# Optimization experiments

Measured on AMD Instinct MI355X. Metric: run time of the kernel, lower is better.

The kernel has to match this reference:

```python
import jax, jax.numpy as jnp
import numpy as np

B, T, INPUT_DIM, EMBED_DIM = 64, 512, 512, 256


def _lstm_dir(x, mask, k, r, b):
    """Masked unidirectional LSTM (Keras semantics: masked steps carry prev h/c).
    x: [B,T,D], mask: [B,T] bool, k: [D,4U], r: [U,4U], b: [4U]. Returns [B,T,U]."""
    Bx = x.shape[0]
    U = r.shape[0]
    # Precompute input projection once for all timesteps (gate order: i,f,g,o)
    xz = jnp.einsum('btd,dk->btk', x, k) + b          # [B,T,4U]
    xz_t = jnp.swapaxes(xz, 0, 1)                     # [T,B,4U]
    mask_t = jnp.swapaxes(mask, 0, 1)                 # [T,B]
    h0 = jnp.zeros((Bx, U), x.dtype)
    c0 = jnp.zeros((Bx, U), x.dtype)

    def step(carry, inp):
        h, c = carry
        z_x, m = inp
        z = z_x + h @ r                               # [B,4U]
        i, f, g, o = jnp.split(z, 4, axis=-1)
        i = jax.nn.sigmoid(i)
        f = jax.nn.sigmoid(f)
        g = jnp.tanh(g)
        o = jax.nn.sigmoid(o)
        c_new = f * c + i * g
        h_new = o * jnp.tanh(c_new)
        m = m[:, None]
        h2 = jnp.where(m, h_new, h)                   # carry state through masked steps
        c2 = jnp.where(m, c_new, c)
        return (h2, c2), h2

    _, hs = jax.lax.scan(step, (h0, c0), (xz_t, mask_t))
    return jnp.swapaxes(hs, 0, 1)                     # [B,T,U]


def _bilstm_sum(x, mask, kf, rf, bf, kb, rb, bb):
    fwd = _lstm_dir(x, mask, kf, rf, bf)
    # Keras Bidirectional: reverse input and mask, run, reverse output back
    bwd = _lstm_dir(x[:, ::-1], mask[:, ::-1], kb, rb, bb)[:, ::-1]
    return fwd + bwd                                  # merge_mode='sum'


def _lstm_params(key, d_in, units):
    k1, k2, k3 = jax.random.split(key, 3)
    kernel = jax.random.normal(k1, (d_in, 4 * units), jnp.float32) / np.sqrt(d_in)
    rec = jax.random.normal(k2, (units, 4 * units), jnp.float32) / np.sqrt(units)
    bias = jnp.concatenate([
        jnp.zeros((units,), jnp.float32),
        jnp.ones((units,), jnp.float32),              # unit_forget_bias
        jnp.zeros((2 * units,), jnp.float32),
    ])
    return kernel, rec, bias


def setup_inputs() -> dict:
    key = jax.random.key(0)
    ks = jax.random.split(key, 6)
    sequences = jax.random.normal(ks[0], (B, T, INPUT_DIM), jnp.float32)
    sizes = jax.random.randint(ks[1], (B,), 0, T, jnp.int32)
    enc_kf, enc_rf, enc_bf = _lstm_params(ks[2], INPUT_DIM, EMBED_DIM)
    enc_kb, enc_rb, enc_bb = _lstm_params(ks[3], INPUT_DIM, EMBED_DIM)
    dec_kf, dec_rf, dec_bf = _lstm_params(ks[4], EMBED_DIM, INPUT_DIM)
    dec_kb, dec_rb, dec_bb = _lstm_params(ks[5], EMBED_DIM, INPUT_DIM)
    return {
        'sequences': sequences, 'sizes': sizes,
        'enc_kf': enc_kf, 'enc_rf': enc_rf, 'enc_bf': enc_bf,
        'enc_kb': enc_kb, 'enc_rb': enc_rb, 'enc_bb': enc_bb,
        'dec_kf': dec_kf, 'dec_rf': dec_rf, 'dec_bf': dec_bf,
        'dec_kb': dec_kb, 'dec_rb': dec_rb, 'dec_bb': dec_bb,
    }


def reference(sequences, sizes,
              enc_kf, enc_rf, enc_bf, enc_kb, enc_rb, enc_bb,
              dec_kf, dec_rf, dec_bf, dec_kb, dec_rb, dec_bb):
    mask = jnp.arange(sequences.shape[1])[None, :] < sizes[:, None]   # [B,T]
    x = _bilstm_sum(sequences, mask, enc_kf, enc_rf, enc_bf, enc_kb, enc_rb, enc_bb)
    x = _bilstm_sum(x, mask, dec_kf, dec_rf, dec_bf, dec_kb, dec_rb, dec_bb)
    return x
```

## Files before the change

### kernel.cpp

```cpp
#include <hip/hip_runtime.h>
#include <stdint.h>

using short8 = __attribute__((ext_vector_type(8))) short;
using f32x4  = __attribute__((ext_vector_type(4))) float;

#define DEV static __device__ __forceinline__

DEV unsigned short f2bf(float f){
  unsigned u = __builtin_bit_cast(unsigned, f);
  u = (u + 0x7FFFu + ((u >> 16) & 1u)) >> 16;
  return (unsigned short)u;
}
DEV float sigm(float x){
  float e = __builtin_amdgcn_exp2f(-1.4426950408889634f * x);
  return __builtin_amdgcn_rcpf(1.0f + e);
}
DEV float tanh_(float x){
  float e = __builtin_amdgcn_exp2f(2.885390081777927f * x);
  return 1.0f - 2.0f * __builtin_amdgcn_rcpf(e + 1.0f);
}


__global__ void k_f32_to_bf16(const float* __restrict__ in, unsigned short* __restrict__ out, int n){
  int stride = gridDim.x * blockDim.x * 4;
  for (int i = (blockIdx.x * blockDim.x + threadIdx.x) * 4; i < n; i += stride){
    float4 v = *(const float4*)(in + i);
    ushort4 o4;
    o4.x = f2bf(v.x); o4.y = f2bf(v.y); o4.z = f2bf(v.z); o4.w = f2bf(v.w);
    *(ushort4*)(out + i) = o4;
  }
}

__global__ void k_add_bf16(const float* __restrict__ a, const float* __restrict__ b,
                           unsigned short* __restrict__ out, int n){
  int stride = gridDim.x * blockDim.x * 4;
  for (int i = (blockIdx.x * blockDim.x + threadIdx.x) * 4; i < n; i += stride){
    float4 va = *(const float4*)(a + i);
    float4 vb = *(const float4*)(b + i);
    ushort4 o4;
    o4.x = f2bf(va.x + vb.x); o4.y = f2bf(va.y + vb.y);
    o4.z = f2bf(va.z + vb.z); o4.w = f2bf(va.w + vb.w);
    *(ushort4*)(out + i) = o4;
  }
}

__global__ void k_add_f32(float* __restrict__ o, const float* __restrict__ b, int n){
  int stride = gridDim.x * blockDim.x * 4;
  for (int i = (blockIdx.x * blockDim.x + threadIdx.x) * 4; i < n; i += stride){
    float4 vo = *(const float4*)(o + i);
    float4 vb = *(const float4*)(b + i);
    vo.x += vb.x; vo.y += vb.y; vo.z += vb.z; vo.w += vb.w;
    *(float4*)(o + i) = vo;
  }
}

__global__ void k_pack(const float* __restrict__ k0, const float* __restrict__ r0,
                       const float* __restrict__ k1, const float* __restrict__ r1,
                       unsigned short* __restrict__ out, int E, int KX, int U){
  int n = 2 * E;
  int stride = gridDim.x * blockDim.x;
  for (int i = blockIdx.x * blockDim.x + threadIdx.x; i < n; i += stride){
    int d = i / E, r = i % E;
    const float* Km = d ? k1 : k0;
    const float* Rm = d ? r1 : r0;
    int j    = r & 7;  int q = r >> 3;
    int lane = q & 63; q >>= 6;
    int nt   = q & 3;  q >>= 2;
    int kt   = q % 6;  q /= 6;
    int w    = q & 3;  int wg = q >> 2;
    int k    = (w*6 + kt)*32 + ((lane >> 4) << 3) + j;
    int col  = nt * U + wg*16 + (lane & 15);
    float v  = (k < KX) ? Km[(size_t)k * (4*U) + col]
                        : Rm[(size_t)(k - KX) * (4*U) + col];
    out[i] = f2bf(v);
  }
}

template<int KX, int U, int WGS>
__global__ __launch_bounds__(256, 1)
void lstm_rec(const unsigned short* __restrict__ xab,
              const unsigned short* __restrict__ packedB,
              const float* __restrict__ bias_f,
              const float* __restrict__ bias_b,
              const int*   __restrict__ sizes,
              unsigned short* __restrict__ hbuf,
              unsigned int*  __restrict__ counters,
              float* __restrict__ out_f,
              float* __restrict__ out_b)
{
  constexpr int KTW = 6;
  constexpr int T   = 512;

  const int tid  = threadIdx.x;
  const int w    = tid >> 6;
  const int lane = tid & 63;
  const int dir  = (blockIdx.x >= WGS) ? 1 : 0;
  const int wg   = dir ? (int)blockIdx.x - WGS : (int)blockIdx.x;

  const unsigned short* pB = packedB + (size_t)dir * ((size_t)WGS*4*KTW*4*512)
                                     + (size_t)((wg*4 + w)*KTW)*4*512;
  unsigned short* hb  = hbuf + (size_t)dir * (2*64*U);
  unsigned int*   cnt = counters + dir * 32;
  const float* bias = dir ? bias_b : bias_f;
  float* outp       = dir ? out_b : out_f;

  const bool has_h = ((w*KTW + KTW - 1) * 32) >= KX;

  short8 bfr[KTW][4];
  #pragma unroll
  for (int kt = 0; kt < KTW; ++kt)
    #pragma unroll
    for (int nt = 0; nt < 4; ++nt)
      bfr[kt][nt] = *(const short8*)(pB + ((kt*4 + nt)*512) + lane*8);

  const int u_l = tid & 15;
  const int rb  = (tid >> 4) * 4;
  const int ug  = wg*16 + u_l;
  float bz[4]; int sz[4];
  #pragma unroll
  for (int g = 0; g < 4; ++g) bz[g] = bias[g*U + ug];
  #pragma unroll
  for (int r = 0; r < 4; ++r) sz[r] = sizes[rb + r];
  float c[4]    = {0.f,0.f,0.f,0.f};
  float hreg[4] = {0.f,0.f,0.f,0.f};

  __shared__ float part[4][64][68];

  const int arow  = lane & 15;
  const int kgrp  = (lane >> 4) * 8;
  const int rquad = (lane >> 4) * 4;

  short8 areg[KTW][4];
  {
    const int t0 = dir ? T - 1 : 0;
    #pragma unroll
    for (int kt = 0; kt < KTW; ++kt){
      const int kg = (w*KTW + kt) * 32;
      if (kg < KX){
        #pragma unroll
        for (int mt = 0; mt < 4; ++mt)
          areg[kt][mt] = *(const short8*)(xab + ((size_t)((mt*16 + arow)*T + t0))*KX + (kg + kgrp));
      }
    }
  }

  for (int s = 0; s < T; ++s){
    const int t   = dir ? (T - 1 - s) : s;
    const int par = s & 1;

    f32x4 acc[4][4];
    #pragma unroll
    for (int mt = 0; mt < 4; ++mt)
      #pragma unroll
      for (int nt = 0; nt < 4; ++nt)
        acc[mt][nt] = (f32x4){0.f, 0.f, 0.f, 0.f};

    #pragma unroll
    for (int kt = 0; kt < KTW; ++kt){
      const int kg = (w*KTW + kt) * 32;
      if (kg < KX){
        #pragma unroll
        for (int mt = 0; mt < 4; ++mt)
          #pragma unroll
          for (int nt = 0; nt < 4; ++nt)
            acc[mt][nt] = __builtin_amdgcn_mfma_f32_16x16x32_bf16(areg[kt][mt], bfr[kt][nt], acc[mt][nt], 0, 0, 0);
      }
    }

    if (s > 0){
      if (has_h){
        const unsigned tgt = (unsigned)WGS * (unsigned)s;
        for (;;){
          unsigned v = __hip_atomic_load(cnt, __ATOMIC_RELAXED, __HIP_MEMORY_SCOPE_AGENT);
          if (v >= tgt) break;
          __builtin_amdgcn_s_sleep(1);
        }
        __builtin_amdgcn_sched_barrier(0);
        #pragma unroll
        for (int kt = 0; kt < KTW; ++kt){
          const int kg = (w*KTW + kt) * 32;
          if (kg >= KX){
            #pragma unroll
            for (int mt = 0; mt < 4; ++mt){
              const unsigned long long* hp = (const unsigned long long*)
                  (hb + (size_t)par*64*U + (size_t)(mt*16 + arow)*U + (kg - KX + kgrp));
              ulonglong2 u;
              u.x = __hip_atomic_load(hp,     __ATOMIC_RELAXED, __HIP_MEMORY_SCOPE_AGENT);
              u.y = __hip_atomic_load(hp + 1, __ATOMIC_RELAXED, __HIP_MEMORY_SCOPE_AGENT);
              areg[kt][mt] = __builtin_bit_cast(short8, u);
            }
          }
        }
        #pragma unroll
        for (int kt = 0; kt < KTW; ++kt){
          const int kg = (w*KTW + kt) * 32;
          if (kg >= KX){
            #pragma unroll
            for (int mt = 0; mt < 4; ++mt)
              #pragma unroll
              for (int nt = 0; nt < 4; ++nt)
                acc[mt][nt] = __builtin_amdgcn_mfma_f32_16x16x32_bf16(areg[kt][mt], bfr[kt][nt], acc[mt][nt], 0, 0, 0);
          }
        }
      }
    }

    #pragma unroll
    for (int mt = 0; mt < 4; ++mt)
      #pragma unroll
      for (int nt = 0; nt < 4; ++nt)
        *(f32x4*)&part[w][nt*16 + arow][mt*16 + rquad] = acc[mt][nt];

    __syncthreads();

    f32x4 zg[4];
    #pragma unroll
    for (int g = 0; g < 4; ++g){
      const int cb = g*16 + u_l;
      f32x4 v = *(const f32x4*)&part[0][cb][rb];
      #pragma unroll
      for (int ww = 1; ww < 4; ++ww)
        v += *(const f32x4*)&part[ww][cb][rb];
      zg[g] = v;
    }

    #pragma unroll
    for (int r = 0; r < 4; ++r){
      float ig = sigm (zg[0][r] + bz[0]);
      float fg = sigm (zg[1][r] + bz[1]);
      float gg = tanh_(zg[2][r] + bz[2]);
      float og = sigm (zg[3][r] + bz[3]);
      float cn = fg * c[r] + ig * gg;
      float hn = og * tanh_(cn);
      bool m  = (t < sz[r]);
      c[r] = m ? cn : c[r];
      float h = m ? hn : hreg[r];
      hreg[r] = h;
      __hip_atomic_store(&hb[(size_t)(par ^ 1)*64*U + (size_t)(rb + r)*U + ug],
                         (unsigned short)f2bf(h),
                         __ATOMIC_RELAXED, __HIP_MEMORY_SCOPE_AGENT);
    }

    __syncthreads();

    if (s != T - 1){
      if (tid == 0) atomicAdd(cnt, 1u);
    }

    #pragma unroll
    for (int r = 0; r < 4; ++r)
      outp[((size_t)(rb + r)*T + t)*U + ug] = hreg[r];

    if (s != T - 1){
      const int tn = dir ? t - 1 : t + 1;
      #pragma unroll
      for (int kt = 0; kt < KTW; ++kt){
        const int kg = (w*KTW + kt) * 32;
        if (kg < KX){
          #pragma unroll
          for (int mt = 0; mt < 4; ++mt)
            areg[kt][mt] = *(const short8*)(xab + ((size_t)((mt*16 + arow)*T + tn))*KX + (kg + kgrp));
        }
      }
    }
  }
}


extern "C" void kernel_launch(void* const* d_in, const int* in_sizes, int n_in,
                              void* d_out, int out_size, void* d_ws, size_t ws_size,
                              hipStream_t stream){
  const float* x      = (const float*)d_in[0];
  const int*   sizes  = (const int*)  d_in[1];
  const float* enc_kf = (const float*)d_in[2];
  const float* enc_rf = (const float*)d_in[3];
  const float* enc_bf = (const float*)d_in[4];
  const float* enc_kb = (const float*)d_in[5];
  const float* enc_rb = (const float*)d_in[6];
  const float* enc_bb = (const float*)d_in[7];
  const float* dec_kf = (const float*)d_in[8];
  const float* dec_rf = (const float*)d_in[9];
  const float* dec_bf = (const float*)d_in[10];
  const float* dec_kb = (const float*)d_in[11];
  const float* dec_rb = (const float*)d_in[12];
  const float* dec_bb = (const float*)d_in[13];
  float* out = (float*)d_out;
  char*  ws  = (char*)d_ws;

  const size_t o_xbf   = 0;
  const size_t o_esum  = o_xbf   + 33554432ull;
  const size_t o_pBe   = o_esum  + 16777216ull;
  const size_t o_pBd   = o_pBe   + 3145728ull;
  const size_t o_hfe   = o_pBd   + 6291456ull;
  const size_t o_hbe   = o_hfe   + 33554432ull;
  const size_t o_hbd   = o_hbe   + 33554432ull;
  const size_t o_hbufe = o_hbd   + 67108864ull;
  const size_t o_hbufd = o_hbufe + 131072ull;
  const size_t o_cnte  = o_hbufd + 262144ull;
  const size_t o_cntd  = o_cnte  + 4096ull;
  const size_t total   = o_cntd  + 4096ull;
  if (ws_size < total) return;

  unsigned short* xbf   = (unsigned short*)(ws + o_xbf);
  unsigned short* esum  = (unsigned short*)(ws + o_esum);
  unsigned short* pBe   = (unsigned short*)(ws + o_pBe);
  unsigned short* pBd   = (unsigned short*)(ws + o_pBd);
  float*          hfe   = (float*)(ws + o_hfe);
  float*          hbe   = (float*)(ws + o_hbe);
  float*          hbd   = (float*)(ws + o_hbd);
  unsigned short* hbufe = (unsigned short*)(ws + o_hbufe);
  unsigned short* hbufd = (unsigned short*)(ws + o_hbufd);
  unsigned int*   cnte  = (unsigned int*)(ws + o_cnte);
  unsigned int*   cntd  = (unsigned int*)(ws + o_cntd);

  hipMemsetAsync(ws + o_cnte, 0, 8192ull, stream);

  k_f32_to_bf16<<<2048, 256, 0, stream>>>(x, xbf, 64*512*512);

  k_pack<<<2048, 256, 0, stream>>>(enc_kf, enc_rf, enc_kb, enc_rb, pBe, 786432, 512, 256);
  k_pack<<<2048, 256, 0, stream>>>(dec_kf, dec_rf, dec_kb, dec_rb, pBd, 1572864, 256, 512);

  lstm_rec<512, 256, 16><<<32, 256, 0, stream>>>(xbf, pBe, enc_bf, enc_bb, sizes,
                                                 hbufe, cnte, hfe, hbe);
  k_add_bf16<<<2048, 256, 0, stream>>>(hfe, hbe, esum, 64*512*256);

  lstm_rec<256, 512, 32><<<64, 256, 0, stream>>>(esum, pBd, dec_bf, dec_bb, sizes,
                                                 hbufd, cntd, out, hbd);
  k_add_f32<<<2048, 256, 0, stream>>>(out, hbd, 64*512*512);
}
```

Before: 5.580 ms.

## Hoist encoder input projection into parallel GEMM and run recurrence per-block with LDS

The encoder's input projection moves out of the recurrent loop into a separate fully parallel MFMA GEMM that writes bf16 gate pre-activations in a transposed layout. The encoder recurrence becomes a new kernel in which each of 8 blocks owns 16 batch rows and one direction, keeps the whole recurrent matrix in registers, and exchanges h through LDS with a local barrier. This removes the cross-workgroup atomic spin-wait per timestep. It costs a large extra workspace buffer (~128MB xz), bf16 rounding of the precomputed gates, and only 8 active CUs during the encoder recurrence. A fallback path keeps the old pipeline when the workspace is too small.

```diff
diff --git a/kernel.cpp b/kernel.cpp
--- a/kernel.cpp
+++ b/kernel.cpp
@@ -3,6 +3,7 @@
 
 using short8 = __attribute__((ext_vector_type(8))) short;
 using f32x4  = __attribute__((ext_vector_type(4))) float;
+typedef unsigned long long ull;
 
 #define DEV static __device__ __forceinline__
 
@@ -11,6 +12,9 @@
   u = (u + 0x7FFFu + ((u >> 16) & 1u)) >> 16;
   return (unsigned short)u;
 }
+DEV float bf2f(unsigned short v){
+  return __builtin_bit_cast(float, ((unsigned)v) << 16);
+}
 DEV float sigm(float x){
   float e = __builtin_amdgcn_exp2f(-1.4426950408889634f * x);
   return __builtin_amdgcn_rcpf(1.0f + e);
@@ -18,6 +22,16 @@
 DEV float tanh_(float x){
   float e = __builtin_amdgcn_exp2f(2.885390081777927f * x);
   return 1.0f - 2.0f * __builtin_amdgcn_rcpf(e + 1.0f);
+}
+DEV void bar_lds(){
+  __builtin_amdgcn_sched_barrier(0);
+  asm volatile("s_waitcnt lgkmcnt(0)" ::: "memory");
+  __builtin_amdgcn_s_barrier();
+  __builtin_amdgcn_sched_barrier(0);
+}
+DEV void colmap_e(int colp, int& g, int& u){
+  int w = colp >> 7, r = colp & 127, nt = r >> 4, l = r & 15;
+  g = nt >> 1; u = w*32 + ((nt & 1) << 4) + l;
 }
 
 
@@ -41,6 +55,20 @@
     o4.x = f2bf(va.x + vb.x); o4.y = f2bf(va.y + vb.y);
     o4.z = f2bf(va.z + vb.z); o4.w = f2bf(va.w + vb.w);
     *(ushort4*)(out + i) = o4;
+  }
+}
+
+__global__ void k_add_bb(const unsigned short* __restrict__ a, const unsigned short* __restrict__ b,
+                         unsigned short* __restrict__ out, int n){
+  int stride = gridDim.x * blockDim.x * 8;
+  for (int i = (blockIdx.x * blockDim.x + threadIdx.x) * 8; i < n; i += stride){
+    short8 va = *(const short8*)(a + i);
+    short8 vb = *(const short8*)(b + i);
+    short8 o;
+    #pragma unroll
+    for (int j = 0; j < 8; ++j)
+      o[j] = (short)f2bf(bf2f((unsigned short)va[j]) + bf2f((unsigned short)vb[j]));
+    *(short8*)(out + i) = o;
   }
 }
 
@@ -76,6 +104,210 @@
   }
 }
 
+__global__ void k_pack_ge(const float* __restrict__ kf, const float* __restrict__ kb,
+                          unsigned short* __restrict__ out){
+  int n = 2 * 524288;
+  int stride = gridDim.x * blockDim.x;
+  for (int i = blockIdx.x * blockDim.x + threadIdx.x; i < n; i += stride){
+    int j    = i & 7;
+    int lane = (i >> 3) & 63;
+    int nt   = (i >> 9) & 3;
+    int kt   = (i >> 11) & 3;
+    int w    = (i >> 13) & 3;
+    int ct   = (i >> 15) & 15;
+    int dir  = i >> 19;
+    int k    = (w*4 + kt)*32 + ((lane >> 4) << 3) + j;
+    int colp = ct*64 + nt*16 + (lane & 15);
+    int g, u; colmap_e(colp, g, u);
+    const float* K = dir ? kb : kf;
+    out[i] = f2bf(K[(size_t)k * 1024 + g*256 + u]);
+  }
+}
+
+__global__ void k_pack_re(const float* __restrict__ rf, const float* __restrict__ rb,
+                          unsigned short* __restrict__ out){
+  int n = 2 * 262144;
+  int stride = gridDim.x * blockDim.x;
+  for (int i = blockIdx.x * blockDim.x + threadIdx.x; i < n; i += stride){
+    int j    = i & 7;
+    int lane = (i >> 3) & 63;
+    int nt   = (i >> 9) & 7;
+    int kt   = (i >> 12) & 7;
+    int w    = (i >> 15) & 7;
+    int dir  = i >> 18;
+    int k    = kt*32 + ((lane >> 4) << 3) + j;
+    int colp = w*128 + nt*16 + (lane & 15);
+    int g, u; colmap_e(colp, g, u);
+    const float* R = dir ? rb : rf;
+    out[i] = f2bf(R[(size_t)k * 1024 + g*256 + u]);
+  }
+}
+
+__global__ __launch_bounds__(256, 1)
+void k_gemm_xz(const unsigned short* __restrict__ xab,
+               const unsigned short* __restrict__ pBg,
+               unsigned short* __restrict__ xzt){
+  const int tid  = threadIdx.x;
+  const int w    = tid >> 6;
+  const int lane = tid & 63;
+  const int ct   = blockIdx.x & 15;
+  const int t    = (blockIdx.x >> 4) & 511;
+  const int dir  = blockIdx.x >> 13;
+
+  short8 bfr[4][4];
+  #pragma unroll
+  for (int kt = 0; kt < 4; ++kt)
+    #pragma unroll
+    for (int nt = 0; nt < 4; ++nt)
+      bfr[kt][nt] = *(const short8*)(pBg + (size_t)((((dir*16 + ct)*4 + w)*4 + kt)*4 + nt)*512 + lane*8);
+
+  const int arow = lane & 15;
+  const int kgrp = (lane >> 4) * 8;
+  const int rquad = (lane >> 4) * 4;
+
+  f32x4 acc[4][4];
+  #pragma unroll
+  for (int mt = 0; mt < 4; ++mt)
+    #pragma unroll
+    for (int nt = 0; nt < 4; ++nt)
+      acc[mt][nt] = (f32x4){0.f,0.f,0.f,0.f};
+
+  #pragma unroll
+  for (int kt = 0; kt < 4; ++kt){
+    const int kg = (w*4 + kt)*32;
+    #pragma unroll
+    for (int mt = 0; mt < 4; ++mt){
+      const int row = mt*16 + arow;
+      short8 a = *(const short8*)(xab + ((size_t)(row*512 + t))*512 + kg + kgrp);
+      #pragma unroll
+      for (int nt = 0; nt < 4; ++nt)
+        acc[mt][nt] = __builtin_amdgcn_mfma_f32_16x16x32_bf16(a, bfr[kt][nt], acc[mt][nt], 0, 0, 0);
+    }
+  }
+
+  __shared__ float part[4][64][68];
+  #pragma unroll
+  for (int mt = 0; mt < 4; ++mt)
+    #pragma unroll
+    for (int nt = 0; nt < 4; ++nt)
+      *(f32x4*)&part[w][nt*16 + arow][mt*16 + rquad] = acc[mt][nt];
+
+  __syncthreads();
+
+  const int cl = tid & 63;
+  const int rq = (tid >> 6) * 16;
+  unsigned short ov[16];
+  #pragma unroll
+  for (int q = 0; q < 4; ++q){
+    f32x4 v = *(const f32x4*)&part[0][cl][rq + q*4];
+    #pragma unroll
+    for (int ww = 1; ww < 4; ++ww)
+      v += *(const f32x4*)&part[ww][cl][rq + q*4];
+    #pragma unroll
+    for (int r = 0; r < 4; ++r) ov[q*4 + r] = f2bf(v[r]);
+  }
+  size_t base = ((size_t)(dir*1024 + ct*64 + cl))*32768 + (size_t)t*64 + rq;
+  *(short8*)(xzt + base)     = *(short8*)&ov[0];
+  *(short8*)(xzt + base + 8) = *(short8*)&ov[8];
+}
+
+__global__ __launch_bounds__(512, 1)
+void k_enc_rec(const unsigned short* __restrict__ xzt,
+               const unsigned short* __restrict__ pBr,
+               const float* __restrict__ bias_f,
+               const float* __restrict__ bias_b,
+               const int*   __restrict__ sizes,
+               unsigned short* __restrict__ out_f,
+               unsigned short* __restrict__ out_b){
+  constexpr int T = 512;
+  const int tid   = threadIdx.x;
+  const int w     = tid >> 6;
+  const int lane  = tid & 63;
+  const int l15   = lane & 15;
+  const int dir   = (int)blockIdx.x >> 2;
+  const int rbase = ((int)blockIdx.x & 3) * 16;
+
+  short8 bfr[8][8];
+  #pragma unroll
+  for (int kt = 0; kt < 8; ++kt)
+    #pragma unroll
+    for (int nt = 0; nt < 8; ++nt)
+      bfr[kt][nt] = *(const short8*)(pBr + (size_t)(((dir*8 + w)*8 + kt)*8 + nt)*512 + lane*8);
+
+  const float* bias = dir ? bias_b : bias_f;
+  unsigned short* outp = dir ? out_b : out_f;
+
+  float bz[2][4];
+  #pragma unroll
+  for (int us = 0; us < 2; ++us){
+    const int u = w*32 + us*16 + l15;
+    #pragma unroll
+    for (int g = 0; g < 4; ++g) bz[us][g] = bias[g*256 + u];
+  }
+  int sz[4];
+  #pragma unroll
+  for (int r2 = 0; r2 < 4; ++r2) sz[r2] = sizes[rbase + (lane >> 4)*4 + r2];
+
+  float c[2][4], hv[2][4];
+  #pragma unroll
+  for (int us = 0; us < 2; ++us)
+    #pragma unroll
+    for (int r2 = 0; r2 < 4; ++r2){ c[us][r2] = 0.f; hv[us][r2] = 0.f; }
+
+  __shared__ unsigned short hl[2][16][264];
+  for (int i = tid; i < 16*264; i += 512) ((unsigned short*)hl[0])[i] = 0;
+  __syncthreads();
+
+  const size_t xzdir = (size_t)dir * 1024 * 32768;
+
+  for (int s = 0; s < T; ++s){
+    const int t   = dir ? (T - 1 - s) : s;
+    const int par = s & 1;
+
+    f32x4 acc[8];
+    #pragma unroll
+    for (int nt = 0; nt < 8; ++nt){
+      const int colp = w*128 + nt*16 + l15;
+      const unsigned short* p = xzt + xzdir + (size_t)colp*32768 + (size_t)t*64 + rbase + ((lane >> 4) << 2);
+      ushort4 xv = *(const ushort4*)p;
+      acc[nt] = (f32x4){bf2f(xv.x), bf2f(xv.y), bf2f(xv.z), bf2f(xv.w)};
+    }
+
+    #pragma unroll
+    for (int kt = 0; kt < 8; ++kt){
+      short8 a = *(const short8*)&hl[par][l15][kt*32 + ((lane >> 4) << 3)];
+      #pragma unroll
+      for (int nt = 0; nt < 8; ++nt)
+        acc[nt] = __builtin_amdgcn_mfma_f32_16x16x32_bf16(a, bfr[kt][nt], acc[nt], 0, 0, 0);
+    }
+
+    #pragma unroll
+    for (int us = 0; us < 2; ++us){
+      const int u = w*32 + us*16 + l15;
+      #pragma unroll
+      for (int r2 = 0; r2 < 4; ++r2){
+        float zi = acc[0 + us][r2] + bz[us][0];
+        float zf = acc[2 + us][r2] + bz[us][1];
+        float zg = acc[4 + us][r2] + bz[us][2];
+        float zo = acc[6 + us][r2] + bz[us][3];
+        float ig = sigm(zi), fg = sigm(zf), gg = tanh_(zg), og = sigm(zo);
+        float cn = fg * c[us][r2] + ig * gg;
+        float hn = og * tanh_(cn);
+        bool m = (t < sz[r2]);
+        c[us][r2] = m ? cn : c[us][r2];
+        float h = m ? hn : hv[us][r2];
+        hv[us][r2] = h;
+        unsigned short hb16 = f2bf(h);
+        const int rloc = (lane >> 4)*4 + r2;
+        hl[par ^ 1][rloc][u] = hb16;
+        outp[((size_t)((rbase + rloc)*512) + t)*256 + u] = hb16;
+      }
+    }
+
+    bar_lds();
+  }
+}
+
 template<int KX, int U, int WGS>
 __global__ __launch_bounds__(256, 1)
 void lstm_rec(const unsigned short* __restrict__ xab,
@@ -130,7 +362,7 @@
   const int kgrp  = (lane >> 4) * 8;
   const int rquad = (lane >> 4) * 4;
 
-  short8 areg[KTW][4];
+  short8 xreg[KTW][4];
   {
     const int t0 = dir ? T - 1 : 0;
     #pragma unroll
@@ -139,7 +371,7 @@
       if (kg < KX){
         #pragma unroll
         for (int mt = 0; mt < 4; ++mt)
-          areg[kt][mt] = *(const short8*)(xab + ((size_t)((mt*16 + arow)*T + t0))*KX + (kg + kgrp));
+          xreg[kt][mt] = *(const short8*)(xab + ((size_t)((mt*16 + arow)*T + t0))*KX + (kg + kgrp));
       }
     }
   }
@@ -163,43 +395,33 @@
         for (int mt = 0; mt < 4; ++mt)
           #pragma unroll
           for (int nt = 0; nt < 4; ++nt)
-            acc[mt][nt] = __builtin_amdgcn_mfma_f32_16x16x32_bf16(areg[kt][mt], bfr[kt][nt], acc[mt][nt], 0, 0, 0);
+            acc[mt][nt] = __builtin_amdgcn_mfma_f32_16x16x32_bf16(xreg[kt][mt], bfr[kt][nt], acc[mt][nt], 0, 0, 0);
       }
     }
 
-    if (s > 0){
-      if (has_h){
-        const unsigned tgt = (unsigned)WGS * (unsigned)s;
-        for (;;){
-          unsigned v = __hip_atomic_load(cnt, __ATOMIC_RELAXED, __HIP_MEMORY_SCOPE_AGENT);
-          if (v >= tgt) break;
-          __builtin_amdgcn_s_sleep(1);
-        }
-        __builtin_amdgcn_sched_barrier(0);
-        #pragma unroll
-        for (int kt = 0; kt < KTW; ++kt){
-          const int kg = (w*KTW + kt) * 32;
-          if (kg >= KX){
+    if (s > 0 && has_h){
+      const unsigned tgt = (unsigned)WGS * (unsigned)s;
+      for (;;){
+        unsigned v = __hip_atomic_load(cnt, __ATOMIC_RELAXED, __HIP_MEMORY_SCOPE_AGENT);
+        if (v >= tgt) break;
+        __builtin_amdgcn_s_sleep(1);
+      }
+      __builtin_amdgcn_sched_barrier(0);
+      #pragma unroll
+      for (int kt = 0; kt < KTW; ++kt){
+        const int kg = (w*KTW + kt) * 32;
+        if (kg >= KX){
+          #pragma unroll
+          for (int mt = 0; mt < 4; ++mt){
+            const ull* hp = (const ull*)
+                (hb + (size_t)par*64*U + (size_t)(mt*16 + arow)*U + (kg - KX + kgrp));
+            ulonglong2 u;
+            u.x = __hip_atomic_load(hp,     __ATOMIC_RELAXED, __HIP_MEMORY_SCOPE_AGENT);
+            u.y = __hip_atomic_load(hp + 1, __ATOMIC_RELAXED, __HIP_MEMORY_SCOPE_AGENT);
+            short8 a = __builtin_bit_cast(short8, u);
             #pragma unroll
-            for (int mt = 0; mt < 4; ++mt){
-              const unsigned long long* hp = (const unsigned long long*)
-                  (hb + (size_t)par*64*U + (size_t)(mt*16 + arow)*U + (kg - KX + kgrp));
-              ulonglong2 u;
-              u.x = __hip_atomic_load(hp,     __ATOMIC_RELAXED, __HIP_MEMORY_SCOPE_AGENT);
-              u.y = __hip_atomic_load(hp + 1, __ATOMIC_RELAXED, __HIP_MEMORY_SCOPE_AGENT);
-              areg[kt][mt] = __builtin_bit_cast(short8, u);
-            }
-          }
-        }
-        #pragma unroll
-        for (int kt = 0; kt < KTW; ++kt){
-          const int kg = (w*KTW + kt) * 32;
-          if (kg >= KX){
-            #pragma unroll
-            for (int mt = 0; mt < 4; ++mt)
-              #pragma unroll
-              for (int nt = 0; nt < 4; ++nt)
-                acc[mt][nt] = __builtin_amdgcn_mfma_f32_16x16x32_bf16(areg[kt][mt], bfr[kt][nt], acc[mt][nt], 0, 0, 0);
+            for (int nt = 0; nt < 4; ++nt)
+              acc[mt][nt] = __builtin_amdgcn_mfma_f32_16x16x32_bf16(a, bfr[kt][nt], acc[mt][nt], 0, 0, 0);
           }
         }
       }
@@ -259,7 +481,7 @@
         if (kg < KX){
           #pragma unroll
           for (int mt = 0; mt < 4; ++mt)
-            areg[kt][mt] = *(const short8*)(xab + ((size_t)((mt*16 + arow)*T + tn))*KX + (kg + kgrp));
+            xreg[kt][mt] = *(const short8*)(xab + ((size_t)((mt*16 + arow)*T + tn))*KX + (kg + kgrp));
         }
       }
     }
@@ -287,44 +509,75 @@
   float* out = (float*)d_out;
   char*  ws  = (char*)d_ws;
 
-  const size_t o_xbf   = 0;
-  const size_t o_esum  = o_xbf   + 33554432ull;
-  const size_t o_pBe   = o_esum  + 16777216ull;
-  const size_t o_pBd   = o_pBe   + 3145728ull;
-  const size_t o_hfe   = o_pBd   + 6291456ull;
-  const size_t o_hbe   = o_hfe   + 33554432ull;
-  const size_t o_hbd   = o_hbe   + 33554432ull;
-  const size_t o_hbufe = o_hbd   + 67108864ull;
-  const size_t o_hbufd = o_hbufe + 131072ull;
-  const size_t o_cnte  = o_hbufd + 262144ull;
-  const size_t o_cntd  = o_cnte  + 4096ull;
-  const size_t total   = o_cntd  + 4096ull;
-  if (ws_size < total) return;
-
-  unsigned short* xbf   = (unsigned short*)(ws + o_xbf);
-  unsigned short* esum  = (unsigned short*)(ws + o_esum);
-  unsigned short* pBe   = (unsigned short*)(ws + o_pBe);
-  unsigned short* pBd   = (unsigned short*)(ws + o_pBd);
-  float*          hfe   = (float*)(ws + o_hfe);
-  float*          hbe   = (float*)(ws + o_hbe);
-  float*          hbd   = (float*)(ws + o_hbd);
-  unsigned short* hbufe = (unsigned short*)(ws + o_hbufe);
-  unsigned short* hbufd = (unsigned short*)(ws + o_hbufd);
-  unsigned int*   cnte  = (unsigned int*)(ws + o_cnte);
-  unsigned int*   cntd  = (unsigned int*)(ws + o_cntd);
-
-  hipMemsetAsync(ws + o_cnte, 0, 8192ull, stream);
-
-  k_f32_to_bf16<<<2048, 256, 0, stream>>>(x, xbf, 64*512*512);
-
-  k_pack<<<2048, 256, 0, stream>>>(enc_kf, enc_rf, enc_kb, enc_rb, pBe, 786432, 512, 256);
-  k_pack<<<2048, 256, 0, stream>>>(dec_kf, dec_rf, dec_kb, dec_rb, pBd, 1572864, 256, 512);
-
-  lstm_rec<512, 256, 16><<<32, 256, 0, stream>>>(xbf, pBe, enc_bf, enc_bb, sizes,
-                                                 hbufe, cnte, hfe, hbe);
-  k_add_bf16<<<2048, 256, 0, stream>>>(hfe, hbe, esum, 64*512*256);
-
-  lstm_rec<256, 512, 32><<<64, 256, 0, stream>>>(esum, pBd, dec_bf, dec_bb, sizes,
-                                                 hbufd, cntd, out, hbd);
-  k_add_f32<<<2048, 256, 0, stream>>>(out, hbd, 64*512*512);
-}
+  const size_t o_xbf  = 0;
+  const size_t o_esum = o_xbf  + 33554432ull;
+  const size_t o_pBd  = o_esum + 16777216ull;
+  const size_t o_ehf  = o_pBd  + 6291456ull;
+  const size_t o_ehb  = o_ehf  + 16777216ull;
+  const size_t o_hbd  = o_ehb  + 16777216ull;
+  const size_t o_hbufd= o_hbd  + 67108864ull;
+  const size_t o_cntd = o_hbufd+ 262144ull;
+  const size_t o_pBg  = o_cntd + 4096ull;
+  const size_t o_pBr  = o_pBg  + 2097152ull;
+  const size_t o_xzt  = o_pBr  + 1048576ull;
+  const size_t NEWTOT = o_xzt  + 134217728ull;
+
+  unsigned short* xbf  = (unsigned short*)(ws + o_xbf);
+  unsigned short* esum = (unsigned short*)(ws + o_esum);
+  unsigned short* pBd  = (unsigned short*)(ws + o_pBd);
+  float*          hbd  = (float*)(ws + o_hbd);
+  unsigned short* hbufd= (unsigned short*)(ws + o_hbufd);
+  unsigned int*   cntd = (unsigned int*)(ws + o_cntd);
+
+  if (ws_size >= NEWTOT){
+    unsigned short* ehf = (unsigned short*)(ws + o_ehf);
+    unsigned short* ehb = (unsigned short*)(ws + o_ehb);
+    unsigned short* pBg = (unsigned short*)(ws + o_pBg);
+    unsigned short* pBr = (unsigned short*)(ws + o_pBr);
+    unsigned short* xzt = (unsigned short*)(ws + o_xzt);
+
+    hipMemsetAsync(ws + o_cntd, 0, 4096ull, stream);
+
+    k_f32_to_bf16<<<2048, 256, 0, stream>>>(x, xbf, 64*512*512);
+    k_pack_ge<<<1024, 256, 0, stream>>>(enc_kf, enc_kb, pBg);
+    k_pack_re<<<512, 256, 0, stream>>>(enc_rf, enc_rb, pBr);
+    k_pack<<<2048, 256, 0, stream>>>(dec_kf, dec_rf, dec_kb, dec_rb, pBd, 1572864, 256, 512);
+
+    k_gemm_xz<<<16384, 256, 0, stream>>>(xbf, pBg, xzt);
+    k_enc_rec<<<8, 512, 0, stream>>>(xzt, pBr, enc_bf, enc_bb, sizes, ehf, ehb);
+    k_add_bb<<<2048, 256, 0, stream>>>(ehf, ehb, esum, 64*512*256);
+    lstm_rec<256, 512, 32><<<64, 256, 0, stream>>>(esum, pBd, dec_bf, dec_bb, sizes,
+                                                   hbufd, cntd, out, hbd);
+    k_add_f32<<<2048, 256, 0, stream>>>(out, hbd, 64*512*512);
+  } else {
+    const size_t f_pBe   = o_pBr;
+    const size_t f_hfe   = o_cntd + 4096ull;
+    const size_t f_hbe   = f_hfe  + 33554432ull;
+    const size_t f_hbufe = f_hbe  + 33554432ull;
+    const size_t f_cnte  = f_hbufe+ 131072ull;
+    const size_t f_pBe2  = f_cnte + 4096ull;
+    const size_t FTOT    = f_pBe2 + 3145728ull;
+    if (ws_size < FTOT) return;
+    (void)f_pBe;
+
+    float* hfe = (float*)(ws + f_hfe);
+    float* hbe = (float*)(ws + f_hbe);
+    unsigned short* hbufe = (unsigned short*)(ws + f_hbufe);
+    unsigned int* cnte = (unsigned int*)(ws + f_cnte);
+    unsigned short* pBe = (unsigned short*)(ws + f_pBe2);
+
+    hipMemsetAsync(ws + o_cntd, 0, 4096ull, stream);
+    hipMemsetAsync(ws + f_cnte, 0, 4096ull, stream);
+
+    k_f32_to_bf16<<<2048, 256, 0, stream>>>(x, xbf, 64*512*512);
+    k_pack<<<2048, 256, 0, stream>>>(enc_kf, enc_rf, enc_kb, enc_rb, pBe, 786432, 512, 256);
+    k_pack<<<2048, 256, 0, stream>>>(dec_kf, dec_rf, dec_kb, dec_rb, pBd, 1572864, 256, 512);
+
+    lstm_rec<512, 256, 16><<<32, 256, 0, stream>>>(xbf, pBe, enc_bf, enc_bb, sizes,
+                                                   hbufe, cnte, hfe, hbe);
+    k_add_bf16<<<2048, 256, 0, stream>>>(hfe, hbe, esum, 64*512*256);
+    lstm_rec<256, 512, 32><<<64, 256, 0, stream>>>(esum, pBd, dec_bf, dec_bb, sizes,
+                                                   hbufd, cntd, out, hbd);
+    k_add_f32<<<2048, 256, 0, stream>>>(out, hbd, 64*512*512);
+  }
+}
```

Result: slower. 8.589 ms (+53.9%).
